# Kernel optimization log

Measured on AMD Instinct MI355X. Metric: run time of the kernel, lower is better.

The kernel has to match this reference:

```python
import jax, jax.numpy as jnp
import numpy as np

S, B, E, H, AW = 4096, 2, 768, 12, 512  # seq, batch, embed, heads, attention_window


def _longformer_local_attn(query, Wq, bq, Wk, bk, Wv, bv):
    # query: [S, B, E] (seq-first, as in the torch module); returns [S, B, E]
    S_, B_, E_ = query.shape
    H_ = H
    D = E_ // H_
    W = AW // 2  # one-sided window (HF Longformer uses window//2 each side)
    x = query.transpose(1, 0, 2)  # [B, S, E]

    q = (x @ Wq + bq).reshape(B_, S_, H_, D) * (1.0 / jnp.sqrt(jnp.asarray(D, x.dtype)))
    k = (x @ Wk + bk).reshape(B_, S_, H_, D)
    v = (x @ Wv + bv).reshape(B_, S_, H_, D)

    nc = S_ // W  # number of query chunks of size W
    # pad keys/values by W on each side so every chunk sees a 3W key window
    kp = jnp.pad(k, ((0, 0), (W, W), (0, 0), (0, 0)))
    vp = jnp.pad(v, ((0, 0), (W, W), (0, 0), (0, 0)))
    # padded-coordinate indices of the 3W key window for each chunk: [nc, 3W]
    idx = jnp.arange(nc)[:, None] * W + jnp.arange(3 * W)[None, :]
    kc = kp[:, idx]  # [B, nc, 3W, H, D]
    vc = vp[:, idx]  # [B, nc, 3W, H, D]
    qc = q.reshape(B_, nc, W, H_, D)

    # banded scores: [B, H, nc, W, 3W]
    scores = jnp.einsum('bcqhd,bckhd->bhcqk', qc, kc)

    # mask: within-band (|rel| <= W) and inside the real sequence
    rel = (jnp.arange(3 * W) - W)[None, :] - jnp.arange(W)[:, None]  # [W, 3W]
    band = jnp.abs(rel) <= W
    abs_k = idx - W  # absolute key index, [nc, 3W]
    in_seq = (abs_k >= 0) & (abs_k < S_)
    mask = band[None, :, :] & in_seq[:, None, :]  # [nc, W, 3W]

    scores = jnp.where(mask[None, None], scores, -jnp.inf)
    attn = jax.nn.softmax(scores, axis=-1)
    out = jnp.einsum('bhcqk,bckhd->bcqhd', attn, vc).reshape(B_, S_, E_)
    return out.transpose(1, 0, 2)  # back to [S, B, E]


def setup_inputs() -> dict:
    key = jax.random.key(0)
    ks = jax.random.split(key, 4)
    scale = 0.02
    return {
        'query': jax.random.normal(ks[0], (S, B, E), jnp.float32),
        'Wq': jax.random.normal(ks[1], (E, E), jnp.float32) * scale,
        'bq': jnp.zeros((E,), jnp.float32),
        'Wk': jax.random.normal(ks[2], (E, E), jnp.float32) * scale,
        'bk': jnp.zeros((E,), jnp.float32),
        'Wv': jax.random.normal(ks[3], (E, E), jnp.float32) * scale,
        'bv': jnp.zeros((E,), jnp.float32),
    }


def reference(query, Wq, bq, Wk, bk, Wv, bv):
    # dropout is identity in eval mode; no global tokens (global mask defaults to zeros)
    return _longformer_local_attn(query, Wq, bq, Wk, bk, Wv, bv)
```

## Files before the change

### kernel.cpp

```cpp
#include <hip/hip_runtime.h>

#define S_ 4096
#define B_ 2
#define E_ 768
#define H_ 12
#define D_ 64

typedef __attribute__((ext_vector_type(8))) short short8;
typedef __attribute__((ext_vector_type(4))) float f32x4;
typedef unsigned short u16;
typedef unsigned int u32;

__device__ __forceinline__ u16 f2bf(float f) {
  union { float f; u32 u; } v; v.f = f;
  u32 r = v.u + 0x7FFFu + ((v.u >> 16) & 1u);
  return (u16)(r >> 16);
}

__device__ __forceinline__ void gl_lds16(const void* g, void* l) {
  __builtin_amdgcn_global_load_lds((const __attribute__((address_space(1))) u32*)g,
                                   (__attribute__((address_space(3))) u32*)l, 16, 0, 0);
}

__global__ __launch_bounds__(256) void k_prep(const float* __restrict__ q,
                                              const float* __restrict__ w0,
                                              const float* __restrict__ w1,
                                              const float* __restrict__ w2,
                                              u16* __restrict__ x,
                                              u16* __restrict__ wt) {
  __shared__ float tile[32][33];
  const int bid = blockIdx.x;
  if (bid < 1728) {
    const int z = bid / 576, r = bid % 576;
    const int k0 = (r / 24) * 32, n0 = (r % 24) * 32;
    const float* w = z == 0 ? w0 : (z == 1 ? w1 : w2);
    const int tx = threadIdx.x & 31, ty = threadIdx.x >> 5;
#pragma unroll
    for (int i = 0; i < 4; i++)
      tile[ty + i * 8][tx] = w[(k0 + ty + i * 8) * 768 + n0 + tx];
    __syncthreads();
    u16* o = wt + (size_t)z * 768 * 768;
#pragma unroll
    for (int i = 0; i < 4; i++)
      o[(n0 + ty + i * 8) * 768 + k0 + tx] = f2bf(tile[tx][ty + i * 8]);
  } else {
    const int m = bid - 1728;
    const int e = threadIdx.x * 4;
    if (e < 768) {
      const int b = m >> 12, s = m & 4095;
      const float4 v = *(const float4*)&q[((s << 1) + b) * 768 + e];
      ushort4 o;
      o.x = f2bf(v.x); o.y = f2bf(v.y); o.z = f2bf(v.z); o.w = f2bf(v.w);
      *(ushort4*)&x[m * 768 + e] = o;
    }
  }
}

__global__ __launch_bounds__(256, 3) void k_gemm_qkv(
    const u16* __restrict__ x, const u16* __restrict__ wt,
    const float* __restrict__ bq, const float* __restrict__ bk,
    const float* __restrict__ bv,
    u16* __restrict__ qb, u16* __restrict__ kb, u16* __restrict__ vt) {
  __shared__ __align__(16) u16 smem[24576];
  const int tid = threadIdx.x;
  const int lane = tid & 63, wave = tid >> 6;
  const int wm = wave >> 1, wn = wave & 1;
  const int l15 = lane & 15, lg = lane >> 4;

  const int bid = blockIdx.x;
  const int xcd = bid & 7, idx = bid >> 3;
  const int m0 = (xcd * 8 + idx / 18) * 128;
  const int n0g = (idx % 18) * 128;
  const int z = n0g / 768, j0 = n0g % 768;
  const u16* wz = wt + (size_t)z * 768 * 768;

  f32x4 acc[4][4] = {};

  auto stage = [&](int buf, int kt) {
#pragma unroll
    for (int c = 0; c < 2; c++) {
      int ci = c * 256 + tid;
      int row = ci >> 2, cp = ci & 3;
      int sc = cp ^ ((row >> 1) & 3);
      gl_lds16(&x[(size_t)(m0 + row) * 768 + kt + sc * 8],
               &smem[buf * 8192 + (c * 256 + wave * 64) * 8]);
    }
#pragma unroll
    for (int c = 0; c < 2; c++) {
      int ci = c * 256 + tid;
      int row = ci >> 2, cp = ci & 3;
      int sc = cp ^ ((row >> 1) & 3);
      gl_lds16(&wz[(size_t)(j0 + row) * 768 + kt + sc * 8],
               &smem[buf * 8192 + 4096 + (c * 256 + wave * 64) * 8]);
    }
  };

  stage(0, 0);
  stage(1, 32);
  const int kc = lg ^ ((l15 >> 1) & 3);
  int cur = 0;
  for (int t = 0; t < 24; t++) {
    if (t < 23) { asm volatile("s_waitcnt vmcnt(4)" ::: "memory"); }
    else       { asm volatile("s_waitcnt vmcnt(0)" ::: "memory"); }
    __builtin_amdgcn_s_barrier();
    __builtin_amdgcn_sched_barrier(0);
    if (t < 22) {
      int st = cur + 2; if (st >= 3) st -= 3;
      stage(st, (t + 2) * 32);
    }
    const int base = cur * 8192;
    short8 a[4], b[4];
#pragma unroll
    for (int mf = 0; mf < 4; mf++)
      a[mf] = *(const short8*)&smem[base + (wm * 64 + mf * 16 + l15) * 32 + kc * 8];
#pragma unroll
    for (int nf = 0; nf < 4; nf++)
      b[nf] = *(const short8*)&smem[base + 4096 + (wn * 64 + nf * 16 + l15) * 32 + kc * 8];
#pragma unroll
    for (int mf = 0; mf < 4; mf++)
#pragma unroll
      for (int nf = 0; nf < 4; nf++)
        acc[mf][nf] = __builtin_amdgcn_mfma_f32_16x16x32_bf16(a[mf], b[nf], acc[mf][nf], 0, 0, 0);
    cur = (cur + 1 == 3) ? 0 : cur + 1;
  }
  __syncthreads();

  u16* ep = &smem[wave * 4608];
  const float* bias_p = (z == 0) ? bq : (z == 1 ? bk : bv);
  const float sc_ = (z == 0) ? 0.125f : 1.0f;
  const int r8 = lane >> 3, cn = lane & 7;
  if (z < 2) {
    u16* t = (z == 0) ? qb : kb;
#pragma unroll
    for (int mf = 0; mf < 4; mf++)
#pragma unroll
      for (int nf = 0; nf < 4; nf++) {
        float bias = bias_p[j0 + wn * 64 + nf * 16 + l15];
#pragma unroll
        for (int r = 0; r < 4; r++)
          ep[(mf * 16 + lg * 4 + r) * 72 + nf * 16 + l15] =
              f2bf((acc[mf][nf][r] + bias) * sc_);
      }
#pragma unroll
    for (int i = 0; i < 8; i++) {
      int rl = i * 8 + r8;
      short8 v = *(const short8*)&ep[rl * 72 + cn * 8];
      *(short8*)&t[(size_t)(m0 + wm * 64 + rl) * 768 + j0 + wn * 64 + cn * 8] = v;
    }
  } else {
#pragma unroll
    for (int nf = 0; nf < 4; nf++) {
      float bias = bias_p[j0 + wn * 64 + nf * 16 + l15];
#pragma unroll
      for (int mf = 0; mf < 4; mf++) {
        ushort4 pk;
        pk.x = f2bf(acc[mf][nf][0] + bias);
        pk.y = f2bf(acc[mf][nf][1] + bias);
        pk.z = f2bf(acc[mf][nf][2] + bias);
        pk.w = f2bf(acc[mf][nf][3] + bias);
        *(ushort4*)&ep[(nf * 16 + l15) * 72 + mf * 16 + lg * 4] = pk;
      }
    }
#pragma unroll
    for (int i = 0; i < 8; i++) {
      int nl = i * 8 + r8;
      int n = j0 + wn * 64 + nl;
      int h = n >> 6, d = n & 63;
      const int bb = m0 >> 12, srow = m0 & 4095;
      short8 v = *(const short8*)&ep[nl * 72 + cn * 8];
      *(short8*)&vt[(((size_t)(bb * 12 + h) * 64 + d) << 12) +
                    srow + wm * 64 + cn * 8] = v;
    }
  }
}

__global__ __launch_bounds__(256) void k_attn(const u16* __restrict__ qb,
                                              const u16* __restrict__ kb,
                                              const u16* __restrict__ vt,
                                              float* __restrict__ out) {
  __shared__ __align__(16) u16 Ks[2][64 * 64];
  __shared__ __align__(16) u16 Vs[2][64 * 64];
  __shared__ __align__(16) u16 pl[4][32 * 72];
  const int tid = threadIdx.x;
  const int lane = tid & 63, wave = tid >> 6;
  const int l15 = lane & 15, lg = lane >> 4;

  const int bid = blockIdx.x;
  const int xcd = bid & 7, i = bid >> 3;
  const int pair = xcd * 3 + (i >> 5);
  const int chunk = i & 31;
  const int b = pair / 12, h = pair % 12;
  const int s0 = chunk * 128;
  const int q0 = s0 + wave * 32;

  short8 qf[2][2];
#pragma unroll
  for (int mf = 0; mf < 2; mf++)
#pragma unroll
    for (int ks = 0; ks < 2; ks++)
      qf[mf][ks] = *(const short8*)&qb[(size_t)((b << 12) + q0 + mf * 16 + l15) * 768 +
                                       h * 64 + ks * 32 + lg * 8];

  f32x4 o[2][4] = {};
  float lsum[2][4] = {};

  int t0 = s0 - 256; if (t0 < 0) t0 = 0;
  int t1 = s0 + 320; if (t1 > 4032) t1 = 4032;

  auto stage = [&](int buf, int kb0) {
#pragma unroll
    for (int c = 0; c < 2; c++) {
      int ci = c * 256 + tid;
      int row = ci >> 3, cc = ci & 7;
      int sc = cc ^ (row & 7);
      gl_lds16(&kb[(size_t)((b << 12) + kb0 + row) * 768 + h * 64 + sc * 8],
               &Ks[buf][(c * 256 + wave * 64) * 8]);
      gl_lds16(&vt[((size_t)((b * 12 + h) * 64 + row) << 12) + kb0 + sc * 8],
               &Vs[buf][(c * 256 + wave * 64) * 8]);
    }
  };

  stage(0, t0);
  __syncthreads();

  int buf = 0;
  for (int kb0 = t0; kb0 <= t1; kb0 += 64) {
    if (kb0 + 64 <= t1) stage(buf ^ 1, kb0 + 64);
    const bool act = (kb0 + 63 >= q0 - 256) && (kb0 <= q0 + 31 + 256);
    if (act) {
      f32x4 sf[2][4] = {};
#pragma unroll
      for (int ks = 0; ks < 2; ks++) {
        short8 bkf[4];
#pragma unroll
        for (int nf = 0; nf < 4; nf++) {
          int row = nf * 16 + l15;
          bkf[nf] = *(const short8*)&Ks[buf][row * 64 + (((ks * 4 + lg) ^ (row & 7)) * 8)];
        }
#pragma unroll
        for (int mf = 0; mf < 2; mf++)
#pragma unroll
          for (int nf = 0; nf < 4; nf++)
            sf[mf][nf] = __builtin_amdgcn_mfma_f32_16x16x32_bf16(qf[mf][ks], bkf[nf], sf[mf][nf], 0, 0, 0);
      }
      if (kb0 < q0 - 192 || kb0 > q0 + 192) {
#pragma unroll
        for (int mf = 0; mf < 2; mf++)
#pragma unroll
          for (int nf = 0; nf < 4; nf++) {
            int kj = kb0 + nf * 16 + l15;
#pragma unroll
            for (int r = 0; r < 4; r++) {
              int qi = q0 + mf * 16 + lg * 4 + r;
              if ((unsigned)(kj - qi + 256) > 512u) sf[mf][nf][r] = -3e38f;
            }
          }
      }
      u16* plw = pl[wave];
#pragma unroll
      for (int mf = 0; mf < 2; mf++)
#pragma unroll
        for (int nf = 0; nf < 4; nf++)
#pragma unroll
          for (int r = 0; r < 4; r++) {
            float p = __expf(sf[mf][nf][r]);
            lsum[mf][r] += p;
            plw[(mf * 16 + lg * 4 + r) * 72 + nf * 16 + l15] = f2bf(p);
          }
      short8 pa[2][2];
#pragma unroll
      for (int mf = 0; mf < 2; mf++)
#pragma unroll
        for (int ks = 0; ks < 2; ks++)
          pa[mf][ks] = *(const short8*)&plw[(mf * 16 + l15) * 72 + ks * 32 + lg * 8];
#pragma unroll
      for (int ks = 0; ks < 2; ks++) {
        short8 bvf[4];
#pragma unroll
        for (int df = 0; df < 4; df++) {
          int row = df * 16 + l15;
          bvf[df] = *(const short8*)&Vs[buf][row * 64 + (((ks * 4 + lg) ^ (row & 7)) * 8)];
        }
#pragma unroll
        for (int mf = 0; mf < 2; mf++)
#pragma unroll
          for (int df = 0; df < 4; df++)
            o[mf][df] = __builtin_amdgcn_mfma_f32_16x16x32_bf16(pa[mf][ks], bvf[df], o[mf][df], 0, 0, 0);
      }
    }
    __syncthreads();
    buf ^= 1;
  }

#pragma unroll
  for (int mf = 0; mf < 2; mf++)
#pragma unroll
    for (int r = 0; r < 4; r++) {
      float l = lsum[mf][r];
      l += __shfl_xor(l, 1); l += __shfl_xor(l, 2);
      l += __shfl_xor(l, 4); l += __shfl_xor(l, 8);
      lsum[mf][r] = l;
    }

#pragma unroll
  for (int mf = 0; mf < 2; mf++)
#pragma unroll
    for (int df = 0; df < 4; df++)
#pragma unroll
      for (int r = 0; r < 4; r++) {
        int s = q0 + mf * 16 + lg * 4 + r;
        out[(size_t)(s * 2 + b) * 768 + h * 64 + df * 16 + l15] =
            o[mf][df][r] / lsum[mf][r];
      }
}

extern "C" void kernel_launch(void* const* d_in, const int* in_sizes, int n_in,
                              void* d_out, int out_size, void* d_ws, size_t ws_size,
                              hipStream_t stream) {
  const float* query = (const float*)d_in[0];
  const float* Wq = (const float*)d_in[1];
  const float* bq = (const float*)d_in[2];
  const float* Wk = (const float*)d_in[3];
  const float* bk = (const float*)d_in[4];
  const float* Wv = (const float*)d_in[5];
  const float* bv = (const float*)d_in[6];
  float* out = (float*)d_out;

  char* ws = (char*)d_ws;
  size_t off = 0;
  auto alloc = [&](size_t bytes) {
    void* p = ws + off;
    off = (off + bytes + 255) & ~(size_t)255;
    return p;
  };
  u16* x  = (u16*)alloc((size_t)8192 * 768 * 2);
  u16* wt = (u16*)alloc((size_t)3 * 768 * 768 * 2);
  u16* qb = (u16*)alloc((size_t)8192 * 768 * 2);
  u16* kb = (u16*)alloc((size_t)8192 * 768 * 2);
  u16* vt = (u16*)alloc((size_t)8192 * 768 * 2);

  hipLaunchKernelGGL(k_prep, dim3(1728 + 8192), dim3(256), 0, stream,
                     query, Wq, Wk, Wv, x, wt);
  hipLaunchKernelGGL(k_gemm_qkv, dim3(1152), dim3(256), 0, stream,
                     x, wt, bq, bk, bv, qb, kb, vt);
  hipLaunchKernelGGL(k_attn, dim3(768), dim3(256), 0, stream, qb, kb, vt, out);
}
```

Measured before the change: 163.5 us.

## Load K/V fragments directly from global memory instead of shared LDS staging

```diff
diff --git a/kernel.cpp b/kernel.cpp
--- a/kernel.cpp
+++ b/kernel.cpp
@@ -178,8 +178,6 @@
                                               const u16* __restrict__ kb,
                                               const u16* __restrict__ vt,
                                               float* __restrict__ out) {
-  __shared__ __align__(16) u16 Ks[2][64 * 64];
-  __shared__ __align__(16) u16 Vs[2][64 * 64];
   __shared__ __align__(16) u16 pl[4][32 * 72];
   const int tid = threadIdx.x;
   const int lane = tid & 63, wave = tid >> 6;
@@ -193,6 +191,9 @@
   const int s0 = chunk * 128;
   const int q0 = s0 + wave * 32;
 
+  const u16* kbase = kb + (size_t)(b << 12) * 768 + h * 64;
+  const u16* vbase = vt + ((size_t)(b * 12 + h) << 18);
+
   short8 qf[2][2];
 #pragma unroll
   for (int mf = 0; mf < 2; mf++)
@@ -204,92 +205,68 @@
   f32x4 o[2][4] = {};
   float lsum[2][4] = {};
 
-  int t0 = s0 - 256; if (t0 < 0) t0 = 0;
-  int t1 = s0 + 320; if (t1 > 4032) t1 = 4032;
-
-  auto stage = [&](int buf, int kb0) {
-#pragma unroll
-    for (int c = 0; c < 2; c++) {
-      int ci = c * 256 + tid;
-      int row = ci >> 3, cc = ci & 7;
-      int sc = cc ^ (row & 7);
-      gl_lds16(&kb[(size_t)((b << 12) + kb0 + row) * 768 + h * 64 + sc * 8],
-               &Ks[buf][(c * 256 + wave * 64) * 8]);
-      gl_lds16(&vt[((size_t)((b * 12 + h) * 64 + row) << 12) + kb0 + sc * 8],
-               &Vs[buf][(c * 256 + wave * 64) * 8]);
-    }
-  };
-
-  stage(0, t0);
-  __syncthreads();
-
-  int buf = 0;
-  for (int kb0 = t0; kb0 <= t1; kb0 += 64) {
-    if (kb0 + 64 <= t1) stage(buf ^ 1, kb0 + 64);
-    const bool act = (kb0 + 63 >= q0 - 256) && (kb0 <= q0 + 31 + 256);
-    if (act) {
-      f32x4 sf[2][4] = {};
-#pragma unroll
-      for (int ks = 0; ks < 2; ks++) {
-        short8 bkf[4];
+  int lo = q0 - 256; if (lo < 0) lo = 0; lo &= ~63;
+  int hi = q0 + 31 + 256; if (hi > S_ - 1) hi = S_ - 1;
+
+  u16* plw = pl[wave];
+  for (int kb0 = lo; kb0 <= hi; kb0 += 64) {
+    short8 bkf[2][4];
+#pragma unroll
+    for (int ks = 0; ks < 2; ks++)
+#pragma unroll
+      for (int nf = 0; nf < 4; nf++)
+        bkf[ks][nf] = *(const short8*)&kbase[(size_t)(kb0 + nf * 16 + l15) * 768 +
+                                             ks * 32 + lg * 8];
+    f32x4 sf[2][4] = {};
+#pragma unroll
+    for (int ks = 0; ks < 2; ks++)
+#pragma unroll
+      for (int mf = 0; mf < 2; mf++)
+#pragma unroll
+        for (int nf = 0; nf < 4; nf++)
+          sf[mf][nf] = __builtin_amdgcn_mfma_f32_16x16x32_bf16(qf[mf][ks], bkf[ks][nf], sf[mf][nf], 0, 0, 0);
+    if (kb0 < q0 - 192 || kb0 > q0 + 192) {
+#pragma unroll
+      for (int mf = 0; mf < 2; mf++)
 #pragma unroll
         for (int nf = 0; nf < 4; nf++) {
-          int row = nf * 16 + l15;
-          bkf[nf] = *(const short8*)&Ks[buf][row * 64 + (((ks * 4 + lg) ^ (row & 7)) * 8)];
+          int kj = kb0 + nf * 16 + l15;
+#pragma unroll
+          for (int r = 0; r < 4; r++) {
+            int qi = q0 + mf * 16 + lg * 4 + r;
+            if ((unsigned)(kj - qi + 256) > 512u) sf[mf][nf][r] = -3e38f;
+          }
         }
-#pragma unroll
-        for (int mf = 0; mf < 2; mf++)
-#pragma unroll
-          for (int nf = 0; nf < 4; nf++)
-            sf[mf][nf] = __builtin_amdgcn_mfma_f32_16x16x32_bf16(qf[mf][ks], bkf[nf], sf[mf][nf], 0, 0, 0);
-      }
-      if (kb0 < q0 - 192 || kb0 > q0 + 192) {
-#pragma unroll
-        for (int mf = 0; mf < 2; mf++)
-#pragma unroll
-          for (int nf = 0; nf < 4; nf++) {
-            int kj = kb0 + nf * 16 + l15;
-#pragma unroll
-            for (int r = 0; r < 4; r++) {
-              int qi = q0 + mf * 16 + lg * 4 + r;
-              if ((unsigned)(kj - qi + 256) > 512u) sf[mf][nf][r] = -3e38f;
-            }
-          }
-      }
-      u16* plw = pl[wave];
+    }
+#pragma unroll
+    for (int mf = 0; mf < 2; mf++)
+#pragma unroll
+      for (int nf = 0; nf < 4; nf++)
+#pragma unroll
+        for (int r = 0; r < 4; r++) {
+          float p = __expf(sf[mf][nf][r]);
+          lsum[mf][r] += p;
+          plw[(mf * 16 + lg * 4 + r) * 72 + nf * 16 + l15] = f2bf(p);
+        }
+    short8 pa[2][2];
+#pragma unroll
+    for (int mf = 0; mf < 2; mf++)
+#pragma unroll
+      for (int ks = 0; ks < 2; ks++)
+        pa[mf][ks] = *(const short8*)&plw[(mf * 16 + l15) * 72 + ks * 32 + lg * 8];
+#pragma unroll
+    for (int ks = 0; ks < 2; ks++) {
+      short8 bvf[4];
+#pragma unroll
+      for (int df = 0; df < 4; df++)
+        bvf[df] = *(const short8*)&vbase[((size_t)(df * 16 + l15) << 12) +
+                                         kb0 + ks * 32 + lg * 8];
 #pragma unroll
       for (int mf = 0; mf < 2; mf++)
 #pragma unroll
-        for (int nf = 0; nf < 4; nf++)
-#pragma unroll
-          for (int r = 0; r < 4; r++) {
-            float p = __expf(sf[mf][nf][r]);
-            lsum[mf][r] += p;
-            plw[(mf * 16 + lg * 4 + r) * 72 + nf * 16 + l15] = f2bf(p);
-          }
-      short8 pa[2][2];
-#pragma unroll
-      for (int mf = 0; mf < 2; mf++)
-#pragma unroll
-        for (int ks = 0; ks < 2; ks++)
-          pa[mf][ks] = *(const short8*)&plw[(mf * 16 + l15) * 72 + ks * 32 + lg * 8];
-#pragma unroll
-      for (int ks = 0; ks < 2; ks++) {
-        short8 bvf[4];
-#pragma unroll
-        for (int df = 0; df < 4; df++) {
-          int row = df * 16 + l15;
-          bvf[df] = *(const short8*)&Vs[buf][row * 64 + (((ks * 4 + lg) ^ (row & 7)) * 8)];
-        }
-#pragma unroll
-        for (int mf = 0; mf < 2; mf++)
-#pragma unroll
-          for (int df = 0; df < 4; df++)
-            o[mf][df] = __builtin_amdgcn_mfma_f32_16x16x32_bf16(pa[mf][ks], bvf[df], o[mf][df], 0, 0, 0);
-      }
-    }
-    __syncthreads();
-    buf ^= 1;
+        for (int df = 0; df < 4; df++)
+          o[mf][df] = __builtin_amdgcn_mfma_f32_16x16x32_bf16(pa[mf][ks], bvf[df], o[mf][df], 0, 0, 0);
+    }
   }
 
 #pragma unroll
```

Result: slower. 181.7 us (+11.1%).
